# Optimization experiments

Hardware: AMD Instinct MI355X
Metric: run time of the kernel (lower is better)

Reference implementation:

```python
import jax, jax.numpy as jnp
import numpy as np

V = 30000   # vocab (from get_word_embedding default)
D = 640     # d_model
L = 6       # num_layers
H = 8       # num_heads
DH = D // H # head dim 80
FF = 4 * D  # ffn hidden 2560
BOS = 1
EOS = 2
LN_EPS = 1e-6


def _ln(x, s, b):
    m = x.mean(-1, keepdims=True)
    v = ((x - m) ** 2).mean(-1, keepdims=True)
    return (x - m) / jnp.sqrt(v + LN_EPS) * s + b


def _get_logits(tokens, seq_len, emb, Wq, bq, Wk, bk, Wv, bv, Wo, bo,
                ln1s, ln1b, W1, b1, W2, b2, ln2s, ln2b, lmW, lmb):
    # tokens: (B,S) int; seq_len: (B,) int
    B, S = tokens.shape
    h = emb[tokens]                                   # (B,S,D), no pos-enc / scaling in source
    look_ahead = jnp.triu(jnp.ones((S, S), jnp.float32), k=1)          # 1 = masked (TF-style)
    pad = (jnp.arange(S)[None, :] >= seq_len[:, None]).astype(jnp.float32)  # (B,S)
    mask = jnp.maximum(look_ahead[None, None, :, :], pad[:, None, None, :])  # (B,1,S,S)

    def layer(h, p):
        wq, bq_, wk, bk_, wv, bv_, wo, bo_, l1s, l1b, w1, b1_, w2, b2_, l2s, l2b = p
        q = (h @ wq + bq_).reshape(B, S, H, DH)
        k = (h @ wk + bk_).reshape(B, S, H, DH)
        v = (h @ wv + bv_).reshape(B, S, H, DH)
        scores = jnp.einsum('bqhd,bkhd->bhqk', q, k) / jnp.sqrt(jnp.float32(DH))
        scores = scores - mask * 1e9
        a = jax.nn.softmax(scores, axis=-1)
        o = jnp.einsum('bhqk,bkhd->bqhd', a, v).reshape(B, S, D) @ wo + bo_
        h = _ln(h + o, l1s, l1b)                      # post-LN residual
        f = jax.nn.relu(h @ w1 + b1_) @ w2 + b2_
        h = _ln(h + f, l2s, l2b)
        return h, None

    h, _ = jax.lax.scan(layer, h, (Wq, bq, Wk, bk, Wv, bv, Wo, bo,
                                   ln1s, ln1b, W1, b1, W2, b2, ln2s, ln2b))
    return h @ lmW + lmb                              # (B,S,V)


def setup_inputs() -> dict:
    key = jax.random.key(0)
    ks = jax.random.split(key, 12)
    std = 0.02

    def n(k, shape):
        return jax.random.normal(k, shape, jnp.float32) * std

    return {
        'initial_words': jax.random.randint(ks[0], (4, 8), 3, V, dtype=jnp.int32),
        'max_length': 32,
        'emb': n(ks[1], (V, D)),
        'Wq': n(ks[2], (L, D, D)), 'bq': jnp.zeros((L, D), jnp.float32),
        'Wk': n(ks[3], (L, D, D)), 'bk': jnp.zeros((L, D), jnp.float32),
        'Wv': n(ks[4], (L, D, D)), 'bv': jnp.zeros((L, D), jnp.float32),
        'Wo': n(ks[5], (L, D, D)), 'bo': jnp.zeros((L, D), jnp.float32),
        'ln1s': jnp.ones((L, D), jnp.float32), 'ln1b': jnp.zeros((L, D), jnp.float32),
        'W1': n(ks[6], (L, D, FF)), 'b1': jnp.zeros((L, FF), jnp.float32),
        'W2': n(ks[7], (L, FF, D)), 'b2': jnp.zeros((L, D), jnp.float32),
        'ln2s': jnp.ones((L, D), jnp.float32), 'ln2b': jnp.zeros((L, D), jnp.float32),
        'lmW': n(ks[8], (D, V)), 'lmb': jnp.zeros((V,), jnp.float32),
    }


def reference(initial_words, max_length, emb, Wq, bq, Wk, bk, Wv, bv, Wo, bo,
              ln1s, ln1b, W1, b1, W2, b2, ln2s, ln2b, lmW, lmb):
    B, init_len = initial_words.shape
    seq_len = jnp.full((B,), max_length, jnp.int32)
    S = max_length + 1  # BOS + max_length slots, as in the torch padding logic
    inp = (jnp.zeros((B, S), jnp.int32)
           .at[:, 0].set(BOS)
           .at[:, 1:1 + init_len].set(initial_words.astype(jnp.int32)))

    def cond(c):
        _inp, cl, tok = c
        return (cl + 1 <= max_length) & jnp.any(tok != EOS)

    def body(c):
        inp, cl, _tok = c
        logits = _get_logits(inp, seq_len, emb, Wq, bq, Wk, bk, Wv, bv, Wo, bo,
                             ln1s, ln1b, W1, b1, W2, b2, ln2s, ln2b, lmW, lmb)
        step_logits = jax.lax.dynamic_index_in_dim(logits, cl, axis=1, keepdims=False)
        tok = jnp.argmax(step_logits, axis=-1).astype(jnp.int32)
        inp = inp.at[:, cl + 1].set(tok)
        return (inp, cl + 1, tok)

    inp, _, _ = jax.lax.while_loop(
        cond, body,
        (inp, jnp.int32(init_len), jnp.full((B,), -100, jnp.int32)))
    return inp[:, 1:]
```

## Files before the change

kernel.cpp:

```cpp
#include <hip/hip_runtime.h>
#include <math.h>

#define B 4
#define SEQ 33
#define MAXLEN 32
#define D 640
#define NH 8
#define DH 80
#define NL 6
#define FF 2560
#define V 30000
#define INITLEN 8
#define NBLK 1024
#define NT 256
#define EOS_TOK 2
#define NPOS_P 9
#define NR_P 36
#define LM_NB 938

#define QKV_N 120
#define AW_B 120
#define RF_B 184
#define F1_B 188
#define F2_B 348
#define RQ_B 428

#define NFLAGS 1024
#define NSLOT 8
#define SLOT_U 16

typedef float f4 __attribute__((ext_vector_type(4)));

struct Par {
  const int* iw;
  const float* emb;
  const float *Wq, *bq, *Wk, *bk, *Wv, *bv, *Wo, *bo;
  const float *ln1s, *ln1b, *W1, *b1, *W2, *b2, *ln2s, *ln2b, *lmW, *lmb;
  int* out;
};

__device__ __align__(256) float g_Kc[(size_t)NL * B * NH * SEQ * DH];
__device__ __align__(256) float g_Vc[(size_t)NL * B * NH * SEQ * DH];
__device__ __align__(256) float g_x[B * D];
__device__ __align__(256) float g_h1[B * D];
__device__ __align__(256) float g_q[D * B];
__device__ __align__(256) float g_kcur[B * D];
__device__ __align__(256) float g_vcur[B * D];
__device__ __align__(256) float g_opart[NH * B * D];
__device__ __align__(256) float g_f1[B * FF];
__device__ __align__(256) float g_f2p[8 * D];
__device__ float g_xp[NR_P * D];
__device__ float g_h1p[NR_P * D];
__device__ float g_qkvpP[(size_t)8 * 1920 * NR_P];
__device__ float g_qP[(size_t)NH * NR_P * DH];
__device__ float g_opartP[(size_t)NH * D * NR_P];
__device__ float g_f1pP[(size_t)8 * FF * NR_P];
__device__ float g_f2pP[(size_t)32 * D * NR_P];
__device__ unsigned long long g_keys[(size_t)NBLK * B];
__device__ int g_tokens[B * SEQ];
__device__ int g_tok[B];
__device__ int g_stop;
__device__ unsigned g_flags[(size_t)NFLAGS * NSLOT * SLOT_U];
__device__ unsigned g_arrive = 0;
__device__ unsigned g_gen = 0;

#define KCIDX(l,b,h,pos,j) (((((size_t)(l)*B+(b))*NH+(h))*SEQ+(pos))*DH+(j))

__device__ __forceinline__ float ldc(const float* p) {
  return __hip_atomic_load(p, __ATOMIC_RELAXED, __HIP_MEMORY_SCOPE_AGENT);
}
__device__ __forceinline__ void stc(float* p, float v) {
  __hip_atomic_store(p, v, __ATOMIC_RELAXED, __HIP_MEMORY_SCOPE_AGENT);
}
__device__ __forceinline__ int ldci(const int* p) {
  return __hip_atomic_load(p, __ATOMIC_RELAXED, __HIP_MEMORY_SCOPE_AGENT);
}
__device__ __forceinline__ void stci(int* p, int v) {
  __hip_atomic_store(p, v, __ATOMIC_RELAXED, __HIP_MEMORY_SCOPE_AGENT);
}
__device__ __forceinline__ void stcu64(unsigned long long* p, unsigned long long v) {
  __hip_atomic_store(p, v, __ATOMIC_RELAXED, __HIP_MEMORY_SCOPE_AGENT);
}
__device__ __forceinline__ void st4c(float* p, f4 v) {
  asm volatile("global_store_dwordx4 %0, %1, off sc1" :: "v"(p), "v"(v) : "memory");
// ... 27 lines not shown
  __syncthreads();
}

__device__ __forceinline__ void stage_done(int idx) {
  asm volatile("s_waitcnt vmcnt(0)" ::: "memory");
  __syncthreads();
  if (threadIdx.x == 0) {
    __hip_atomic_fetch_add(
        &g_flags[((size_t)idx * NSLOT + (blockIdx.x & (NSLOT - 1))) * SLOT_U],
        1u, __ATOMIC_RELAXED, __HIP_MEMORY_SCOPE_AGENT);
  }
}

__device__ __forceinline__ void stage_wait(int idx, unsigned cnt) {
  if (threadIdx.x < 64) {
    const unsigned* base = &g_flags[(size_t)idx * NSLOT * SLOT_U];
    int spins = 0;
    for (;;) {
      unsigned v = 0u;
      if (threadIdx.x < NSLOT)
        v = __hip_atomic_load(base + (size_t)threadIdx.x * SLOT_U,
                              __ATOMIC_RELAXED, __HIP_MEMORY_SCOPE_AGENT);
      #pragma unroll
      for (int o = 4; o > 0; o >>= 1) v += __shfl_down(v, o, 64);
      v = __shfl(v, 0, 64);
      if (v >= cnt) break;
      if (spins < 16)      __builtin_amdgcn_s_sleep(1);
      else if (spins < 96) __builtin_amdgcn_s_sleep(16);
      else                 __builtin_amdgcn_s_sleep(127);
      ++spins;
    }
  }
  __syncthreads();
  asm volatile("" ::: "memory");
}

__device__ __forceinline__ float bred_sum(float v, float* s_red) {
  #pragma unroll
  for (int o = 32; o > 0; o >>= 1) v += __shfl_down(v, o, 64);
  __syncthreads();
  if ((threadIdx.x & 63) == 0) s_red[threadIdx.x >> 6] = v;
  __syncthreads();
  return s_red[0] + s_red[1] + s_red[2] + s_red[3];
}

__device__ void ln_inplace(float* row, const float* gam, const float* bet, float* s_red) {
  float ps = 0.f;
  for (int d = threadIdx.x; d < D; d += NT) ps += row[d];
  const float m = bred_sum(ps, s_red) * (1.0f / 640.0f);
  float pv = 0.f;
  for (int d = threadIdx.x; d < D; d += NT) { float t = row[d] - m; pv += t * t; }
  const float var = bred_sum(pv, s_red) * (1.0f / 640.0f);
  const float rstd = 1.0f / sqrtf(var + 1e-6f);
  for (int d = threadIdx.x; d < D; d += NT)
    row[d] = (row[d] - m) * rstd * gam[d] + bet[d];
  __syncthreads();
}


__device__ void st_QKV(const Par& p, int l, int t, float* s_x, float* s_t, float* s_r) {
  const int tid = threadIdx.x;
  const int cg = blockIdx.x;
  const int m = cg / 40, colm0 = (cg % 40) * 16;
  if (l == 0) {
    for (int i = tid; i < 640; i += NT) {
      const int b = i / 160, c4 = i % 160;
      const int tok = ldci(&g_tok[b]);
      *(f4*)&s_x[b * 640 + c4 * 4] = *(const f4*)&p.emb[(size_t)tok * D + c4 * 4];
    }
  } else {
    f4 xb[3];
    #pragma unroll
    for (int i = 0; i < 3; ++i) {
      const int idx = tid + i * NT;
      if (idx < 640) ld4c_issue(xb[i], &g_x[idx * 4]);
    }
    wait_vm();
    #pragma unroll
    for (int i = 0; i < 3; ++i) {
      const int idx = tid + i * NT;
      if (idx < 640) *(f4*)&s_x[idx * 4] = xb[i];
    }
  }
  __syncthreads();
  if (l == 0 && cg == 0) {
    for (int i = tid; i < 640; i += NT)
      st4c(&g_x[i * 4], *(f4*)&s_x[i * 4]);
  }
  const int ds = tid >> 4, c = tid & 15;
  const float* Wb = (m == 0 ? p.Wq : m == 1 ? p.Wk : p.Wv)
                    + (size_t)l * D * D + colm0 + c;
  float a0 = 0, a1 = 0, a2 = 0, a3 = 0;
  for (int kb = 0; kb < 40; kb += 8) {
    float w[8];
    #pragma unroll
    for (int j = 0; j < 8; ++j)
      w[j] = Wb[(size_t)(ds + (kb + j) * 16) * D];
    #pragma unroll
    for (int j = 0; j < 8; ++j) {
      const int dd = ds + (kb + j) * 16;
      a0 = fmaf(s_x[dd],        w[j], a0);
      a1 = fmaf(s_x[640 + dd],  w[j], a1);
      a2 = fmaf(s_x[1280 + dd], w[j], a2);
      a3 = fmaf(s_x[1920 + dd], w[j], a3);
    }
  }
  { f4 av = { a0, a1, a2, a3 }; *(f4*)&s_t[c * 68 + ds * 4] = av; }
  __syncthreads();
  if (tid < 64) {
    const int c2 = tid >> 2, b = tid & 3;
    float v = 0.f;
    #pragma unroll
    for (int d2 = 0; d2 < 16; ++d2) v += s_t[c2 * 68 + d2 * 4 + b];
    v += (m == 0 ? p.bq : m == 1 ? p.bk : p.bv)[(size_t)l * D + colm0 + c2];
    s_r[c2 * 4 + b] = v;
  }
  __syncthreads();
  if (m == 0) {
    if (tid < 16) {
      f4 v = { s_r[tid * 4], s_r[tid * 4 + 1], s_r[tid * 4 + 2], s_r[tid * 4 + 3] };
      st4c(&g_q[(size_t)(colm0 + tid) * 4], v);
    }
  } else {
    const int h = colm0 / 80, j0 = colm0 % 80;
    if (tid < 16) {
      const int cq = tid & 3, b = tid >> 2;
      f4 v = { s_r[(cq*4+0)*4+b], s_r[(cq*4+1)*4+b], s_r[(cq*4+2)*4+b], s_r[(cq*4+3)*4+b] };
      float* cache = (m == 1) ? g_Kc : g_Vc;
      st4c(&cache[KCIDX(l, b, h, t, j0 + cq * 4)], v);
      float* cur = (m == 1) ? g_kcur : g_vcur;
      st4c(&cur[b * D + colm0 + cq * 4], v);
    }
  }
}

__device__ void st_AW(const Par& p, int l, int pos,
                      float* s_q, float* s_k, float* s_v, float* s_o, float* s_sc, float* s_wo) {
  const int idx = blockIdx.x - AW_B, h = idx >> 3, c = idx & 7, tid = threadIdx.x;
  {
    f4 vq, vk, vv;
    if (tid < 80) {
      ld4c_issue(vq, &g_q[(size_t)(h * 80 + tid) * 4]);
      const int b = tid / 20, q4 = tid % 20;
      ld4c_issue(vk, &g_kcur[b * D + h * 80 + q4 * 4]);
      ld4c_issue(vv, &g_vcur[b * D + h * 80 + q4 * 4]);
    }
    wait_vm();
    if (tid < 80) {
      s_q[0*80+tid] = vq.x; s_q[80+tid] = vq.y; s_q[160+tid] = vq.z; s_q[240+tid] = vq.w;
      const int b = tid / 20, q4 = tid % 20;
      *(f4*)&s_k[b * 80 + q4 * 4] = vk;
      *(f4*)&s_v[b * 80 + q4 * 4] = vv;
    }
  }
  __syncthreads();
  const int nk = pos + 1;
  for (int task = tid; task < 4 * nk; task += NT) {
    const int b = task / nk, kp = task % nk;
    const float* qq = s_q + b * 80;
    float sd = 0.f;
    if (kp == pos) {
      const float* kk = s_k + b * 80;
      for (int j = 0; j < 80; ++j) sd += qq[j] * kk[j];
    } else {
      const f4* kk = (const f4*)&g_Kc[KCIDX(l, b, h, kp, 0)];
      #pragma unroll
      for (int j4 = 0; j4 < 20; ++j4) {
        f4 k4 = kk[j4];
        sd += qq[j4*4+0]*k4.x + qq[j4*4+1]*k4.y + qq[j4*4+2]*k4.z + qq[j4*4+3]*k4.w;
      }
    }
    s_sc[b * 33 + kp] = sd / 8.94427190999915878564f;
  }
  __syncthreads();
  if (tid < 4) {
    const int b = tid;
    float m = -1e30f;
    for (int k = 0; k < nk; ++k) m = fmaxf(m, s_sc[b * 33 + k]);
    float sum = 0.f;
    for (int k = 0; k < nk; ++k) { float e = expf(s_sc[b * 33 + k] - m); s_sc[b * 33 + k] = e; sum += e; }
    s_sc[132 + b] = 1.0f / sum;
  }
  __syncthreads();
  if (tid < 80) {
    const int b = tid / 20, j4 = tid % 20;
    f4 acc = { 0.f, 0.f, 0.f, 0.f };
    for (int kp = 0; kp < pos; ++kp) {
      f4 v = *(const f4*)&g_Vc[KCIDX(l, b, h, kp, j4 * 4)];
      const float wgt = s_sc[b * 33 + kp];
      acc.x += wgt * v.x; acc.y += wgt * v.y; acc.z += wgt * v.z; acc.w += wgt * v.w;
    }
    {
      f4 v = *(const f4*)&s_v[b * 80 + j4 * 4];
      const float wgt = s_sc[b * 33 + pos];
      acc.x += wgt * v.x; acc.y += wgt * v.y; acc.z += wgt * v.z; acc.w += wgt * v.w;
    }
    const float r = s_sc[132 + b];
    f4 o = { acc.x * r, acc.y * r, acc.z * r, acc.w * r };
    *(f4*)&s_o[b * 80 + j4 * 4] = o;
  }
  __syncthreads();
  if (tid < 240) {
    const int j = tid % 80, sub = tid / 80;
    const int col = c * 80 + j;
    const int d0 = sub * 27, d1 = (sub == 2) ? 80 : d0 + 27;
    const float* Wo = p.Wo + (size_t)l * D * D + col;
    float a0 = 0, a1 = 0, a2 = 0, a3 = 0;
    #pragma unroll 9
    for (int dd = d0; dd < d1; ++dd) {
      const float w = Wo[(size_t)(h * 80 + dd) * D];
      a0 += s_o[0*80+dd] * w; a1 += s_o[80+dd] * w;
      a2 += s_o[160+dd] * w; a3 += s_o[240+dd] * w;
    }
    float* tp = s_wo + (j * 3 + sub) * 4;
    tp[0] = a0; tp[1] = a1; tp[2] = a2; tp[3] = a3;
  }
  __syncthreads();
  if (tid < 80) {
    const int b = tid / 20, cq = tid % 20;
    f4 v;
    #pragma unroll
    for (int i = 0; i < 4; ++i) {
      const int j = cq * 4 + i;
      v[i] = s_wo[(j*3+0)*4+b] + s_wo[(j*3+1)*4+b] + s_wo[(j*3+2)*4+b];
    }
    st4c(&g_opart[((size_t)h * 4 + b) * D + c * 80 + cq * 4], v);
  }
}

__device__ void st_RF(const Par& p, int l, float* s_row, float* s_red) {
  const int b = blockIdx.x - RF_B, tid = threadIdx.x;
  f4 xv, ov[8];
  if (tid < 160) {
    ld4c_issue(xv, &g_x[b * D + tid * 4]);
    #pragma unroll
    for (int h = 0; h < 8; ++h)
      ld4c_issue(ov[h], &g_opart[((size_t)h * 4 + b) * D + tid * 4]);
  }
  wait_vm();
  if (tid < 160) {
    const float* bo = p.bo + (size_t)l * D + tid * 4;
    f4 a;
    a.x = xv.x + bo[0]; a.y = xv.y + bo[1]; a.z = xv.z + bo[2]; a.w = xv.w + bo[3];
    #pragma unroll
    for (int h = 0; h < 8; ++h) {
      a.x += ov[h].x; a.y += ov[h].y; a.z += ov[h].z; a.w += ov[h].w;
    }
    *(f4*)&s_row[tid * 4] = a;
  }
  __syncthreads();
  ln_inplace(s_row, p.ln1s + (size_t)l * D, p.ln1b + (size_t)l * D, s_red);
  if (tid < 160) st4c(&g_h1[b * D + tid * 4], *(f4*)&s_row[tid * 4]);
}

__device__ void st_F1(const Par& p, int l, float* s_x, float* s_t, float* s_r) {
  const int tid = threadIdx.x;
  const int cg = blockIdx.x - F1_B;
  const int col0 = cg * 16;
  f4 hb[3];
  #pragma unroll
  for (int i = 0; i < 3; ++i) {
    const int idx = tid + i * NT;
    if (idx < 640) ld4c_issue(hb[i], &g_h1[idx * 4]);
  }
  wait_vm();
  #pragma unroll
  for (int i = 0; i < 3; ++i) {
    const int idx = tid + i * NT;
    if (idx < 640) *(f4*)&s_x[idx * 4] = hb[i];
  }
  __syncthreads();
  const int ds = tid >> 4, c = tid & 15;
  const float* Wb = p.W1 + (size_t)l * D * FF + col0 + c;
  float a0 = 0, a1 = 0, a2 = 0, a3 = 0;
  for (int kb = 0; kb < 40; kb += 8) {
    float w[8];
    #pragma unroll
    for (int j = 0; j < 8; ++j)
      w[j] = Wb[(size_t)(ds + (kb + j) * 16) * FF];
    #pragma unroll
    for (int j = 0; j < 8; ++j) {
      const int dd = ds + (kb + j) * 16;
      a0 = fmaf(s_x[dd],        w[j], a0);
      a1 = fmaf(s_x[640 + dd],  w[j], a1);
      a2 = fmaf(s_x[1280 + dd], w[j], a2);
      a3 = fmaf(s_x[1920 + dd], w[j], a3);
    }
  }
  { f4 av = { a0, a1, a2, a3 }; *(f4*)&s_t[c * 68 + ds * 4] = av; }
  __syncthreads();
  if (tid < 64) {
    const int c2 = tid >> 2, b = tid & 3;
    float v = 0.f;
    #pragma unroll
    for (int d2 = 0; d2 < 16; ++d2) v += s_t[c2 * 68 + d2 * 4 + b];
    v += p.b1[(size_t)l * FF + col0 + c2];
    s_r[c2 * 4 + b] = fmaxf(v, 0.f);
  }
  __syncthreads();
  if (tid < 16) {
    const int cq = tid & 3, b = tid >> 2;
    f4 v = { s_r[(cq*4+0)*4+b], s_r[(cq*4+1)*4+b], s_r[(cq*4+2)*4+b], s_r[(cq*4+3)*4+b] };
    st4c(&g_f1[(size_t)b * FF + col0 + cq * 4], v);
  }
}

__device__ void st_F2(const Par& p, int l, float* s_f, float* s_t, float* s_r) {
  const int idx = blockIdx.x - F2_B, tid = threadIdx.x;
  const int hf = idx / 40, cg = idx % 40;
  const int col0 = cg * 16;
  f4 fb[5];
  #pragma unroll
  for (int i = 0; i < 5; ++i) {
    const int ii = tid + i * NT;
    const int b = ii / 320, fo = ii % 320;
    ld4c_issue(fb[i], &g_f1[(size_t)b * FF + hf * 1280 + fo * 4]);
  }
  wait_vm();
  #pragma unroll
  for (int i = 0; i < 5; ++i) {
    const int ii = tid + i * NT;
    const int b = ii / 320, fo = ii % 320;
    *(f4*)&s_f[b * 1280 + fo * 4] = fb[i];
  }
  __syncthreads();
  const int ds = tid >> 4, c = tid & 15;
  const float* Wb = p.W2 + (size_t)l * FF * D + (size_t)hf * 1280 * D + col0 + c;
  float a0 = 0, a1 = 0, a2 = 0, a3 = 0;
  for (int kb = 0; kb < 80; kb += 16) {
    float w[16];
    #pragma unroll
    for (int j = 0; j < 16; ++j)
      w[j] = Wb[(size_t)(ds + (kb + j) * 16) * D];
    #pragma unroll
    for (int j = 0; j < 16; ++j) {
      const int dl = ds + (kb + j) * 16;
      a0 = fmaf(s_f[dl],        w[j], a0);
      a1 = fmaf(s_f[1280 + dl], w[j], a1);
      a2 = fmaf(s_f[2560 + dl], w[j], a2);
      a3 = fmaf(s_f[3840 + dl], w[j], a3);
    }
  }
  { f4 av = { a0, a1, a2, a3 }; *(f4*)&s_t[c * 68 + ds * 4] = av; }
  __syncthreads();
  if (tid < 64) {
    const int c2 = tid >> 2, b = tid & 3;
    float v = 0.f;
    #pragma unroll
    for (int d2 = 0; d2 < 16; ++d2) v += s_t[c2 * 68 + d2 * 4 + b];
    s_r[c2 * 4 + b] = v;
  }
  __syncthreads();
  if (tid < 16) {
    const int cq = tid & 3, b = tid >> 2;
    f4 v = { s_r[(cq*4+0)*4+b], s_r[(cq*4+1)*4+b], s_r[(cq*4+2)*4+b], s_r[(cq*4+3)*4+b] };
    st4c(&g_f2p[((size_t)hf * 4 + b) * D + col0 + cq * 4], v);
  }
}

__device__ void st_RQ(const Par& p, int lprev, float* s_row, float* s_red) {
  const int b = blockIdx.x - RQ_B, tid = threadIdx.x;
  f4 hv, f0, f1v;
  if (tid < 160) {
    ld4c_issue(hv,  &g_h1[b * D + tid * 4]);
    ld4c_issue(f0,  &g_f2p[(size_t)(0 * 4 + b) * D + tid * 4]);
    ld4c_issue(f1v, &g_f2p[(size_t)(1 * 4 + b) * D + tid * 4]);
  }
  wait_vm();
  if (tid < 160) {
    const float* b2 = p.b2 + (size_t)lprev * D + tid * 4;
    f4 a;
    a.x = hv.x + f0.x + f1v.x + b2[0];
    a.y = hv.y + f0.y + f1v.y + b2[1];
    a.z = hv.z + f0.z + f1v.z + b2[2];
    a.w = hv.w + f0.w + f1v.w + b2[3];
    *(f4*)&s_row[tid * 4] = a;
  }
  __syncthreads();
  ln_inplace(s_row, p.ln2s + (size_t)lprev * D, p.ln2b + (size_t)lprev * D, s_red);
  if (tid < 160) st4c(&g_x[b * D + tid * 4], *(f4*)&s_row[tid * 4]);
}

__device__ void st_LM(const Par& p, float* s_xf, float* s_part, unsigned long long* s_key) {
  const int bid = blockIdx.x, tid = threadIdx.x;
  f4 xb[3];
  #pragma unroll
  for (int i = 0; i < 3; ++i) {
    const int idx = tid + i * NT;
    if (idx < 640) ld4c_issue(xb[i], &g_x[idx * 4]);
  }
  wait_vm();
  #pragma unroll
  for (int i = 0; i < 3; ++i) {
    const int idx = tid + i * NT;
    if (idx < 640) *(f4*)&s_xf[idx * 4] = xb[i];
  }
  __syncthreads();
  const int sg = tid >> 5, cj = tid & 31;
  const int col = bid * 32 + cj;
  float a0 = 0, a1 = 0, a2 = 0, a3 = 0;
  if (col < V) {
    const float* W = p.lmW + (size_t)sg * 80 * V + col;
    for (int kb = 0; kb < 80; kb += 16) {
      float w[16];
      #pragma unroll
      for (int j = 0; j < 16; ++j) w[j] = W[(size_t)(kb + j) * V];
      #pragma unroll
      for (int j = 0; j < 16; ++j) {
        const int d = sg * 80 + kb + j;
        a0 = fmaf(s_xf[d],        w[j], a0);
        a1 = fmaf(s_xf[640 + d],  w[j], a1);
        a2 = fmaf(s_xf[1280 + d], w[j], a2);
        a3 = fmaf(s_xf[1920 + d], w[j], a3);
      }
    }
  }
  float* t = s_part + (sg * 32 + cj) * 4;
  t[0] = a0; t[1] = a1; t[2] = a2; t[3] = a3;
  __syncthreads();
  if (tid < 128) {
    const int cj2 = tid >> 2, b = tid & 3, col2 = bid * 32 + cj2;
    unsigned long long key = 0ull;
    if (col2 < V) {
      float a = p.lmb[col2];
      #pragma unroll
      for (int sg2 = 0; sg2 < 8; ++sg2) a += s_part[(sg2 * 32 + cj2) * 4 + b];
      unsigned u = __float_as_uint(a);
      u = (u & 0x80000000u) ? ~u : (u | 0x80000000u);
      key = ((unsigned long long)u << 32) | (unsigned)(V - col2);
    }
    s_key[cj2 * 4 + b] = key;
  }
  __syncthreads();
  if (tid < 4) {
    unsigned long long k0 = 0ull;
    for (int cj2 = 0; cj2 < 32; ++cj2) {
      const unsigned long long k = s_key[cj2 * 4 + tid];
      if (k > k0) k0 = k;
    }
    stcu64(&g_keys[(size_t)bid * B + tid], k0);
  }
// ... 26 lines not shown
    s = mk64(kb3.x,kb3.y); if (s>m2) m2=s;  s = mk64(kb3.z,kb3.w); if (s>m3) m3=s;
  }
  #pragma unroll
  for (int o = 32; o > 0; o >>= 1) {
    unsigned long long s;
    s = __shfl_down(m0, o, 64); if (s > m0) m0 = s;
    s = __shfl_down(m1, o, 64); if (s > m1) m1 = s;
    s = __shfl_down(m2, o, 64); if (s > m2) m2 = s;
    s = __shfl_down(m3, o, 64); if (s > m3) m3 = s;
  }
  if ((tid & 63) == 0) {
    const int w = tid >> 6;
    s_k64[w * 4 + 0] = m0; s_k64[w * 4 + 1] = m1;
    s_k64[w * 4 + 2] = m2; s_k64[w * 4 + 3] = m3;
  }
  __syncthreads();
  if (tid == 0) {
    #pragma unroll
    for (int b = 0; b < B; ++b) {
      unsigned long long k0 = s_k64[b];
      #pragma unroll
      for (int w = 1; w < 4; ++w) if (s_k64[w * 4 + b] > k0) k0 = s_k64[w * 4 + b];
      const int tok = V - (int)(unsigned)(k0 & 0xFFFFFFFFull);
      stci(&g_tok[b], tok);
      stci(&g_tokens[b * SEQ + t + 1], tok);
      s_ctl[b] = tok;
    }
    int stop = (t == MAXLEN - 1) ? 1 : 0;
    if (s_ctl[0] == EOS_TOK && s_ctl[1] == EOS_TOK &&
        s_ctl[2] == EOS_TOK && s_ctl[3] == EOS_TOK) stop = 1;
    stci(&g_stop, stop);
  }
}


__device__ void st_Qp(const Par& p, int l, float* s_a) {
  const int idx = blockIdx.x, tid = threadIdx.x;
  const int h = idx / 24, rem = idx % 24, s = rem / 3, rg = rem % 3;
  const int r0 = rg * 12, d0 = s * 80;
  for (int i = tid; i < 960; i += NT) {
    const int ri = i / 80, dd = i % 80;
    s_a[i] = ldc(&g_xp[(r0 + ri) * D + d0 + dd]);
  }
  __syncthreads();
  if (tid < 240) {
    const int m = tid / 80, j = tid % 80, col = h * 80 + j;
    const float* W = (m == 0 ? p.Wq : m == 1 ? p.Wk : p.Wv) + (size_t)l * D * D + col;
    float acc[12];
    #pragma unroll
    for (int ri = 0; ri < 12; ++ri) acc[ri] = 0.f;
    for (int dd = 0; dd < 80; ++dd) {
      const float w = W[(size_t)(d0 + dd) * D];
      #pragma unroll
      for (int ri = 0; ri < 12; ++ri) acc[ri] += s_a[ri * 80 + dd] * w;
// ... 153 lines not shown
__device__ void st_RQp(const Par& p, int l, float* s_row, float* s_red) {
  const int r = blockIdx.x, tid = threadIdx.x;
  for (int col = tid; col < D; col += NT) {
    float a = ldc(&g_h1p[r * D + col]) + p.b2[(size_t)l * D + col];
    #pragma unroll 8
    for (int c = 0; c < 32; ++c) a += ldc(&g_f2pP[((size_t)c * D + col) * NR_P + r]);
    s_row[col] = a;
  }
  __syncthreads();
  ln_inplace(s_row, p.ln2s + (size_t)l * D, p.ln2b + (size_t)l * D, s_red);
  for (int col = tid; col < D; col += NT) stc(&g_xp[r * D + col], s_row[col]);
}

__device__ void st_RLp(const Par& p, float* s_row, float* s_red) {
  const int b = blockIdx.x, r = 32 + b, tid = threadIdx.x;
  for (int col = tid; col < D; col += NT) {
    float a = ldc(&g_h1p[r * D + col]) + p.b2[(size_t)(NL - 1) * D + col];
    #pragma unroll 8
    for (int c = 0; c < 32; ++c) a += ldc(&g_f2pP[((size_t)c * D + col) * NR_P + r]);
    s_row[col] = a;
  }
  __syncthreads();
  ln_inplace(s_row, p.ln2s + (size_t)(NL - 1) * D, p.ln2b + (size_t)(NL - 1) * D, s_red);
  for (int col = tid; col < D; col += NT) stc(&g_x[b * D + col], s_row[col]);
}

__global__ __launch_bounds__(NT, 4) void tfgen(Par p) {
  __shared__ float s_pool[6400];
  __shared__ float s_red[8];
  __shared__ unsigned long long s_key[128];
  __shared__ int s_ctl[8];

  const int bid = blockIdx.x, tid = threadIdx.x;
  int ep = 0;

  {
    unsigned* f = g_flags + (size_t)bid * NSLOT * SLOT_U;
    for (int i = tid; i < NSLOT * SLOT_U; i += NT) f[i] = 0u;
  }
  if (bid < NR_P) {
    const int pos = bid >> 2, b = bid & 3;
    const int tk = (pos == 0) ? 1 : p.iw[b * INITLEN + pos - 1];
    for (int d = tid; d < D; d += NT) stc(&g_xp[bid * D + d], p.emb[(size_t)tk * D + d]);
  }
  if (bid == NBLK - 1) {
    for (int i = tid; i < B * SEQ; i += NT) {
      const int b = i / SEQ, pos = i % SEQ;
// ... 16 lines not shown
    const int eA1 = ep++;
    if (bid >= 192 && bid < 224) { stage_wait(eQ, 192); st_AWp1(p, l); stage_done(eA1); }
    const int eA2 = ep++;
    if (bid >= 224 && bid < 256) { stage_wait(eA1, 32); st_AWp2(p, l, ps_a, ps_b, ps_c); stage_done(eA2); }
    const int eRF = ep++;
    if (bid < NR_P) { stage_wait(eA2, 32); st_RFp(p, l, ps_x, s_red); stage_done(eRF); }
    const int eF1 = ep++;
    if (bid < 240) { stage_wait(eRF, 36); st_F1p(p, l, ps_a); stage_done(eF1); }
    const int eF2 = ep++;
    if (bid >= 240 && bid < 336) { stage_wait(eF1, 240); st_F2p(p, l, ps_c); stage_done(eF2); }
    eF2last = eF2;
    if (l < NL - 1) {
      eRQ = ep++;
      if (bid < NR_P) { stage_wait(eF2, 96); st_RQp(p, l, ps_x, s_red); stage_done(eRQ); }
    }
  }

  for (int t = INITLEN;; ++t) {
    int eCTL;
    if (t == INITLEN) {
      const int eRLp = ep++;
      if (bid < 4) { stage_wait(eF2last, 96); st_RLp(p, s_pool, s_red); stage_done(eRLp); }
      const int eLM = ep++;
      if (bid < LM_NB) { stage_wait(eRLp, 4); st_LM(p, s_pool, s_pool + 2560, s_key); stage_done(eLM); }
      eCTL = ep++;
      if (bid == NBLK - 1) { stage_wait(eLM, LM_NB); st_CTL(t, s_key, s_ctl); stage_done(eCTL); }
    } else {
      int eRQd = -1, eF2s = -1;
      for (int l = 0; l < NL; ++l) {
        const int eQKV = ep++;
        if (bid < QKV_N) {
          if (l > 0) stage_wait(eRQd, 4);
          st_QKV(p, l, t, s_pool, s_pool + 2560, s_pool + 3648);
          stage_done(eQKV);
        }
        const int eAW = ep++;
        if (bid >= AW_B && bid < RF_B) {
          stage_wait(eQKV, QKV_N);
          st_AW(p, l, t, s_pool, s_pool + 320, s_pool + 640, s_pool + 960,
                s_pool + 1280, s_pool + 1440);
          stage_done(eAW);
        }
        const int eRF = ep++;
        if (bid >= RF_B && bid < F1_B) { stage_wait(eAW, 64); st_RF(p, l, s_pool, s_red); stage_done(eRF); }
        const int eF1 = ep++;
        if (bid >= F1_B && bid < F2_B) {
          stage_wait(eRF, 4);
          st_F1(p, l, s_pool, s_pool + 2560, s_pool + 3648);
          stage_done(eF1);
        }
        eF2s = ep++;
        if (bid >= F2_B && bid < RQ_B) {
          stage_wait(eF1, 160);
          st_F2(p, l, s_pool, s_pool + 5120, s_pool + 6208);
          stage_done(eF2s);
        }
        if (l < NL - 1) {
          eRQd = ep++;
          if (bid >= RQ_B && bid < RQ_B + 4) { stage_wait(eF2s, 80); st_RQ(p, l, s_pool, s_red); stage_done(eRQd); }
        }
      }
      const int eRL = ep++;
      if (bid >= RQ_B && bid < RQ_B + 4) { stage_wait(eF2s, 80); st_RQ(p, NL - 1, s_pool, s_red); stage_done(eRL); }
      const int eLM = ep++;
      if (bid < LM_NB) { stage_wait(eRL, 4); st_LM(p, s_pool, s_pool + 2560, s_key); stage_done(eLM); }
      eCTL = ep++;
      if (bid == NBLK - 1) { stage_wait(eLM, LM_NB); st_CTL(t, s_key, s_ctl); stage_done(eCTL); }
    }
    stage_wait(eCTL, 1);
    if (tid == 0) s_ctl[0] = ldci(&g_stop);
    __syncthreads();
    if (s_ctl[0]) break;
  }

  if (bid == 0) {
    for (int i = tid; i < B * MAXLEN; i += NT) {
      const int b = i >> 5, j = i & 31;
      p.out[i] = ldci(&g_tokens[b * SEQ + j + 1]);
    }
  }
}

extern "C" void kernel_launch(void* const* d_in, const int* in_sizes, int n_in,
                              void* d_out, int out_size, void* d_ws, size_t ws_size,
                              hipStream_t stream)
{
  (void)in_sizes; (void)n_in; (void)out_size; (void)d_ws; (void)ws_size;
  Par p;
  p.iw   = (const int*)  d_in[0];
  p.emb  = (const float*)d_in[2];
  p.Wq   = (const float*)d_in[3];  p.bq   = (const float*)d_in[4];
  p.Wk   = (const float*)d_in[5];  p.bk   = (const float*)d_in[6];
  p.Wv   = (const float*)d_in[7];  p.bv   = (const float*)d_in[8];
  p.Wo   = (const float*)d_in[9];  p.bo   = (const float*)d_in[10];
  p.ln1s = (const float*)d_in[11]; p.ln1b = (const float*)d_in[12];
// ... 14 lines not shown
```

Measured before the change: 18.13 ms.

## Version intermediate buffers per step and fold residual LayerNorm into QKV stage

Every intermediate activation buffer is now indexed by (step, layer), so no slot is reused across stages. Reads can then be plain loads instead of coherent atomic loads. The separate residual+LayerNorm (RQ) stage between layers is removed: each QKV block redoes the residual sum and LayerNorm itself, which drops one grid-wide stage wait per layer at the cost of redundant per-block work. The attention stage now reads the current K/V from the cache instead of separate buffers, flag slots grow to 32, and the weight-load unroll changes to 20. Plain loads on freshly written global data could read stale cached values if coherence is not guaranteed.

```diff
diff --git a/kernel.cpp b/kernel.cpp
--- a/kernel.cpp
+++ b/kernel.cpp
@@ -23,11 +23,13 @@
 #define RF_B 184
 #define F1_B 188
 #define F2_B 348
-#define RQ_B 428
+#define RL_B 428
 
 #define NFLAGS 1024
-#define NSLOT 8
+#define NSLOT 32
 #define SLOT_U 16
+
+#define VER(t,l) ((size_t)((t) * NL + (l)))
 
 typedef float f4 __attribute__((ext_vector_type(4)));
 
@@ -41,14 +43,15 @@
 
 __device__ __align__(256) float g_Kc[(size_t)NL * B * NH * SEQ * DH];
 __device__ __align__(256) float g_Vc[(size_t)NL * B * NH * SEQ * DH];
-__device__ __align__(256) float g_x[B * D];
-__device__ __align__(256) float g_h1[B * D];
-__device__ __align__(256) float g_q[D * B];
-__device__ __align__(256) float g_kcur[B * D];
-__device__ __align__(256) float g_vcur[B * D];
-__device__ __align__(256) float g_opart[NH * B * D];
-__device__ __align__(256) float g_f1[B * FF];
-__device__ __align__(256) float g_f2p[8 * D];
+__device__ __align__(256) float g_xv[(size_t)SEQ * NL * 2560];
+__device__ __align__(256) float g_h1v[(size_t)SEQ * NL * 2560];
+__device__ __align__(256) float g_qv[(size_t)SEQ * NL * 2560];
+__device__ __align__(256) float g_opartv[(size_t)SEQ * NL * 20480];
+__device__ __align__(256) float g_f1v[(size_t)SEQ * NL * 10240];
+__device__ __align__(256) float g_f2v[(size_t)SEQ * NL * 5120];
+__device__ __align__(256) float g_xlm[(size_t)SEQ * 2560];
+__device__ __align__(256) int   g_tokv[SEQ * 64];
+__device__ __align__(256) int   g_stopv[SEQ * 64];
 __device__ float g_xp[NR_P * D];
 __device__ float g_h1p[NR_P * D];
 __device__ float g_qkvpP[(size_t)8 * 1920 * NR_P];
@@ -58,8 +61,6 @@
 __device__ float g_f2pP[(size_t)32 * D * NR_P];
 __device__ unsigned long long g_keys[(size_t)NBLK * B];
 __device__ int g_tokens[B * SEQ];
-__device__ int g_tok[B];
-__device__ int g_stop;
 __device__ unsigned g_flags[(size_t)NFLAGS * NSLOT * SLOT_U];
 __device__ unsigned g_arrive = 0;
 __device__ unsigned g_gen = 0;
@@ -133,7 +134,7 @@
         v = __hip_atomic_load(base + (size_t)threadIdx.x * SLOT_U,
                               __ATOMIC_RELAXED, __HIP_MEMORY_SCOPE_AGENT);
       #pragma unroll
-      for (int o = 4; o > 0; o >>= 1) v += __shfl_down(v, o, 64);
+      for (int o = 16; o > 0; o >>= 1) v += __shfl_down(v, o, 64);
       v = __shfl(v, 0, 64);
       if (v >= cnt) break;
       if (spins < 16)      __builtin_amdgcn_s_sleep(1);
@@ -173,47 +174,63 @@
   const int tid = threadIdx.x;
   const int cg = blockIdx.x;
   const int m = cg / 40, colm0 = (cg % 40) * 16;
+  const int w = tid >> 6, lane = tid & 63;
   if (l == 0) {
-    for (int i = tid; i < 640; i += NT) {
-      const int b = i / 160, c4 = i % 160;
-      const int tok = ldci(&g_tok[b]);
-      *(f4*)&s_x[b * 640 + c4 * 4] = *(const f4*)&p.emb[(size_t)tok * D + c4 * 4];
-    }
+    const int tok = g_tokv[t * 64 + w];
+    for (int c4 = lane; c4 < 160; c4 += 64)
+      *(f4*)&s_x[w * 640 + c4 * 4] = *(const f4*)&p.emb[(size_t)tok * D + c4 * 4];
   } else {
-    f4 xb[3];
-    #pragma unroll
-    for (int i = 0; i < 3; ++i) {
-      const int idx = tid + i * NT;
-      if (idx < 640) ld4c_issue(xb[i], &g_x[idx * 4]);
-    }
-    wait_vm();
-    #pragma unroll
-    for (int i = 0; i < 3; ++i) {
-      const int idx = tid + i * NT;
-      if (idx < 640) *(f4*)&s_x[idx * 4] = xb[i];
-    }
-  }
-  __syncthreads();
-  if (l == 0 && cg == 0) {
+    const size_t ver = VER(t, l - 1);
+    const float* h1 = g_h1v + ver * 2560 + w * 640;
+    const float* fa = g_f2v + ver * 5120 + w * 640;
+    const float* fb = g_f2v + ver * 5120 + 2560 + w * 640;
+    const float* b2 = p.b2 + (size_t)(l - 1) * D;
+    for (int c4 = lane; c4 < 160; c4 += 64) {
+      f4 a = *(const f4*)&h1[c4 * 4];
+      f4 b = *(const f4*)&fa[c4 * 4];
+      f4 c = *(const f4*)&fb[c4 * 4];
+      const float* bb = b2 + c4 * 4;
+      f4 s = { a.x + b.x + c.x + bb[0], a.y + b.y + c.y + bb[1],
+               a.z + b.z + c.z + bb[2], a.w + b.w + c.w + bb[3] };
+      *(f4*)&s_x[w * 640 + c4 * 4] = s;
+    }
+    float ps = 0.f;
+    for (int i = lane; i < D; i += 64) ps += s_x[w * 640 + i];
+    #pragma unroll
+    for (int o = 32; o > 0; o >>= 1) ps += __shfl_xor(ps, o, 64);
+    const float mean = ps * (1.0f / 640.0f);
+    float pv = 0.f;
+    for (int i = lane; i < D; i += 64) { float d = s_x[w * 640 + i] - mean; pv += d * d; }
+    #pragma unroll
+    for (int o = 32; o > 0; o >>= 1) pv += __shfl_xor(pv, o, 64);
+    const float rstd = 1.0f / sqrtf(pv * (1.0f / 640.0f) + 1e-6f);
+    const float* gam = p.ln2s + (size_t)(l - 1) * D;
+    const float* bet = p.ln2b + (size_t)(l - 1) * D;
+    for (int i = lane; i < D; i += 64)
+      s_x[w * 640 + i] = (s_x[w * 640 + i] - mean) * rstd * gam[i] + bet[i];
+  }
+  __syncthreads();
+  if (cg == 0) {
+    const size_t xo = VER(t, l) * 2560;
     for (int i = tid; i < 640; i += NT)
-      st4c(&g_x[i * 4], *(f4*)&s_x[i * 4]);
+      st4c(&g_xv[xo + (size_t)i * 4], *(f4*)&s_x[i * 4]);
   }
   const int ds = tid >> 4, c = tid & 15;
   const float* Wb = (m == 0 ? p.Wq : m == 1 ? p.Wk : p.Wv)
                     + (size_t)l * D * D + colm0 + c;
   float a0 = 0, a1 = 0, a2 = 0, a3 = 0;
-  for (int kb = 0; kb < 40; kb += 8) {
-    float w[8];
-    #pragma unroll
-    for (int j = 0; j < 8; ++j)
-      w[j] = Wb[(size_t)(ds + (kb + j) * 16) * D];
-    #pragma unroll
-    for (int j = 0; j < 8; ++j) {
+  #pragma unroll
+  for (int kb = 0; kb < 40; kb += 20) {
+    float wv[20];
+    #pragma unroll
+    for (int j = 0; j < 20; ++j) wv[j] = Wb[(size_t)(ds + (kb + j) * 16) * D];
+    #pragma unroll
+    for (int j = 0; j < 20; ++j) {
       const int dd = ds + (kb + j) * 16;
-      a0 = fmaf(s_x[dd],        w[j], a0);
-      a1 = fmaf(s_x[640 + dd],  w[j], a1);
-      a2 = fmaf(s_x[1280 + dd], w[j], a2);
-      a3 = fmaf(s_x[1920 + dd], w[j], a3);
+      a0 = fmaf(s_x[dd],        wv[j], a0);
+      a1 = fmaf(s_x[640 + dd],  wv[j], a1);
+      a2 = fmaf(s_x[1280 + dd], wv[j], a2);
+      a3 = fmaf(s_x[1920 + dd], wv[j], a3);
     }
   }
   { f4 av = { a0, a1, a2, a3 }; *(f4*)&s_t[c * 68 + ds * 4] = av; }
@@ -230,7 +247,7 @@
   if (m == 0) {
     if (tid < 16) {
       f4 v = { s_r[tid * 4], s_r[tid * 4 + 1], s_r[tid * 4 + 2], s_r[tid * 4 + 3] };
-      st4c(&g_q[(size_t)(colm0 + tid) * 4], v);
+      st4c(&g_qv[VER(t, l) * 2560 + (size_t)(colm0 + tid) * 4], v);
     }
   } else {
     const int h = colm0 / 80, j0 = colm0 % 80;
@@ -239,47 +256,29 @@
       f4 v = { s_r[(cq*4+0)*4+b], s_r[(cq*4+1)*4+b], s_r[(cq*4+2)*4+b], s_r[(cq*4+3)*4+b] };
       float* cache = (m == 1) ? g_Kc : g_Vc;
       st4c(&cache[KCIDX(l, b, h, t, j0 + cq * 4)], v);
-      float* cur = (m == 1) ? g_kcur : g_vcur;
-      st4c(&cur[b * D + colm0 + cq * 4], v);
-    }
-  }
-}
-
-__device__ void st_AW(const Par& p, int l, int pos,
-                      float* s_q, float* s_k, float* s_v, float* s_o, float* s_sc, float* s_wo) {
+    }
+  }
+}
+
+__device__ void st_AW(const Par& p, int l, int t,
+                      float* s_q, float* s_sc, float* s_o, float* s_wo) {
   const int idx = blockIdx.x - AW_B, h = idx >> 3, c = idx & 7, tid = threadIdx.x;
-  {
-    f4 vq, vk, vv;
-    if (tid < 80) {
-      ld4c_issue(vq, &g_q[(size_t)(h * 80 + tid) * 4]);
-      const int b = tid / 20, q4 = tid % 20;
-      ld4c_issue(vk, &g_kcur[b * D + h * 80 + q4 * 4]);
-      ld4c_issue(vv, &g_vcur[b * D + h * 80 + q4 * 4]);
-    }
-    wait_vm();
-    if (tid < 80) {
-      s_q[0*80+tid] = vq.x; s_q[80+tid] = vq.y; s_q[160+tid] = vq.z; s_q[240+tid] = vq.w;
-      const int b = tid / 20, q4 = tid % 20;
-      *(f4*)&s_k[b * 80 + q4 * 4] = vk;
-      *(f4*)&s_v[b * 80 + q4 * 4] = vv;
-    }
-  }
-  __syncthreads();
-  const int nk = pos + 1;
+  const size_t qo = VER(t, l) * 2560;
+  if (tid < 80) {
+    f4 q = *(const f4*)&g_qv[qo + (size_t)(h * 80 + tid) * 4];
+    s_q[tid] = q.x; s_q[80 + tid] = q.y; s_q[160 + tid] = q.z; s_q[240 + tid] = q.w;
+  }
+  __syncthreads();
+  const int nk = t + 1;
   for (int task = tid; task < 4 * nk; task += NT) {
     const int b = task / nk, kp = task % nk;
     const float* qq = s_q + b * 80;
+    const f4* kk = (const f4*)&g_Kc[KCIDX(l, b, h, kp, 0)];
     float sd = 0.f;
-    if (kp == pos) {
-      const float* kk = s_k + b * 80;
-      for (int j = 0; j < 80; ++j) sd += qq[j] * kk[j];
-    } else {
-      const f4* kk = (const f4*)&g_Kc[KCIDX(l, b, h, kp, 0)];
-      #pragma unroll
-      for (int j4 = 0; j4 < 20; ++j4) {
-        f4 k4 = kk[j4];
-        sd += qq[j4*4+0]*k4.x + qq[j4*4+1]*k4.y + qq[j4*4+2]*k4.z + qq[j4*4+3]*k4.w;
-      }
+    #pragma unroll
+    for (int j4 = 0; j4 < 20; ++j4) {
+      f4 k4 = kk[j4];
+      sd += qq[j4*4+0]*k4.x + qq[j4*4+1]*k4.y + qq[j4*4+2]*k4.z + qq[j4*4+3]*k4.w;
     }
     s_sc[b * 33 + kp] = sd / 8.94427190999915878564f;
   }
@@ -296,14 +295,9 @@
   if (tid < 80) {
     const int b = tid / 20, j4 = tid % 20;
     f4 acc = { 0.f, 0.f, 0.f, 0.f };
-    for (int kp = 0; kp < pos; ++kp) {
+    for (int kp = 0; kp < nk; ++kp) {
       f4 v = *(const f4*)&g_Vc[KCIDX(l, b, h, kp, j4 * 4)];
       const float wgt = s_sc[b * 33 + kp];
-      acc.x += wgt * v.x; acc.y += wgt * v.y; acc.z += wgt * v.z; acc.w += wgt * v.w;
-    }
-    {
-      f4 v = *(const f4*)&s_v[b * 80 + j4 * 4];
-      const float wgt = s_sc[b * 33 + pos];
       acc.x += wgt * v.x; acc.y += wgt * v.y; acc.z += wgt * v.z; acc.w += wgt * v.w;
     }
     const float r = s_sc[132 + b];
@@ -335,67 +329,56 @@
       const int j = cq * 4 + i;
       v[i] = s_wo[(j*3+0)*4+b] + s_wo[(j*3+1)*4+b] + s_wo[(j*3+2)*4+b];
     }
-    st4c(&g_opart[((size_t)h * 4 + b) * D + c * 80 + cq * 4], v);
-  }
-}
-
-__device__ void st_RF(const Par& p, int l, float* s_row, float* s_red) {
+    st4c(&g_opartv[VER(t, l) * 20480 + (size_t)(h * 4 + b) * 640 + c * 80 + cq * 4], v);
+  }
+}
+
+__device__ void st_RF(const Par& p, int l, int t, float* s_row, float* s_red) {
   const int b = blockIdx.x - RF_B, tid = threadIdx.x;
-  f4 xv, ov[8];
+  const size_t ver = VER(t, l);
   if (tid < 160) {
-    ld4c_issue(xv, &g_x[b * D + tid * 4]);
-    #pragma unroll
-    for (int h = 0; h < 8; ++h)
-      ld4c_issue(ov[h], &g_opart[((size_t)h * 4 + b) * D + tid * 4]);
-  }
-  wait_vm();
-  if (tid < 160) {
+    f4 xv = *(const f4*)&g_xv[ver * 2560 + (size_t)b * 640 + tid * 4];
     const float* bo = p.bo + (size_t)l * D + tid * 4;
     f4 a;
     a.x = xv.x + bo[0]; a.y = xv.y + bo[1]; a.z = xv.z + bo[2]; a.w = xv.w + bo[3];
     #pragma unroll
     for (int h = 0; h < 8; ++h) {
-      a.x += ov[h].x; a.y += ov[h].y; a.z += ov[h].z; a.w += ov[h].w;
+      f4 ov = *(const f4*)&g_opartv[ver * 20480 + (size_t)(h * 4 + b) * 640 + tid * 4];
+      a.x += ov.x; a.y += ov.y; a.z += ov.z; a.w += ov.w;
     }
     *(f4*)&s_row[tid * 4] = a;
   }
   __syncthreads();
   ln_inplace(s_row, p.ln1s + (size_t)l * D, p.ln1b + (size_t)l * D, s_red);
-  if (tid < 160) st4c(&g_h1[b * D + tid * 4], *(f4*)&s_row[tid * 4]);
-}
-
-__device__ void st_F1(const Par& p, int l, float* s_x, float* s_t, float* s_r) {
+  if (tid < 160) st4c(&g_h1v[ver * 2560 + (size_t)b * 640 + tid * 4], *(f4*)&s_row[tid * 4]);
+}
+
+__device__ void st_F1(const Par& p, int l, int t, float* s_x, float* s_t, float* s_r) {
   const int tid = threadIdx.x;
   const int cg = blockIdx.x - F1_B;
   const int col0 = cg * 16;
-  f4 hb[3];
+  const size_t ver = VER(t, l);
   #pragma unroll
   for (int i = 0; i < 3; ++i) {
     const int idx = tid + i * NT;
-    if (idx < 640) ld4c_issue(hb[i], &g_h1[idx * 4]);
-  }
-  wait_vm();
-  #pragma unroll
-  for (int i = 0; i < 3; ++i) {
-    const int idx = tid + i * NT;
-    if (idx < 640) *(f4*)&s_x[idx * 4] = hb[i];
+    if (idx < 640) *(f4*)&s_x[idx * 4] = *(const f4*)&g_h1v[ver * 2560 + (size_t)idx * 4];
   }
   __syncthreads();
   const int ds = tid >> 4, c = tid & 15;
   const float* Wb = p.W1 + (size_t)l * D * FF + col0 + c;
   float a0 = 0, a1 = 0, a2 = 0, a3 = 0;
-  for (int kb = 0; kb < 40; kb += 8) {
-    float w[8];
-    #pragma unroll
-    for (int j = 0; j < 8; ++j)
-      w[j] = Wb[(size_t)(ds + (kb + j) * 16) * FF];
-    #pragma unroll
-    for (int j = 0; j < 8; ++j) {
+  #pragma unroll
+  for (int kb = 0; kb < 40; kb += 20) {
+    float wv[20];
+    #pragma unroll
+    for (int j = 0; j < 20; ++j) wv[j] = Wb[(size_t)(ds + (kb + j) * 16) * FF];
+    #pragma unroll
+    for (int j = 0; j < 20; ++j) {
       const int dd = ds + (kb + j) * 16;
-      a0 = fmaf(s_x[dd],        w[j], a0);
-      a1 = fmaf(s_x[640 + dd],  w[j], a1);
-      a2 = fmaf(s_x[1280 + dd], w[j], a2);
-      a3 = fmaf(s_x[1920 + dd], w[j], a3);
+      a0 = fmaf(s_x[dd],        wv[j], a0);
+      a1 = fmaf(s_x[640 + dd],  wv[j], a1);
+      a2 = fmaf(s_x[1280 + dd], wv[j], a2);
+      a3 = fmaf(s_x[1920 + dd], wv[j], a3);
     }
   }
   { f4 av = { a0, a1, a2, a3 }; *(f4*)&s_t[c * 68 + ds * 4] = av; }
@@ -412,44 +395,38 @@
   if (tid < 16) {
     const int cq = tid & 3, b = tid >> 2;
     f4 v = { s_r[(cq*4+0)*4+b], s_r[(cq*4+1)*4+b], s_r[(cq*4+2)*4+b], s_r[(cq*4+3)*4+b] };
-    st4c(&g_f1[(size_t)b * FF + col0 + cq * 4], v);
-  }
-}
-
-__device__ void st_F2(const Par& p, int l, float* s_f, float* s_t, float* s_r) {
+    st4c(&g_f1v[ver * 10240 + (size_t)b * 2560 + col0 + cq * 4], v);
+  }
+}
+
+__device__ void st_F2(const Par& p, int l, int t, float* s_f, float* s_t, float* s_r) {
   const int idx = blockIdx.x - F2_B, tid = threadIdx.x;
   const int hf = idx / 40, cg = idx % 40;
   const int col0 = cg * 16;
-  f4 fb[5];
+  const size_t ver = VER(t, l);
   #pragma unroll
   for (int i = 0; i < 5; ++i) {
     const int ii = tid + i * NT;
     const int b = ii / 320, fo = ii % 320;
-    ld4c_issue(fb[i], &g_f1[(size_t)b * FF + hf * 1280 + fo * 4]);
-  }
-  wait_vm();
-  #pragma unroll
-  for (int i = 0; i < 5; ++i) {
-    const int ii = tid + i * NT;
-    const int b = ii / 320, fo = ii % 320;
-    *(f4*)&s_f[b * 1280 + fo * 4] = fb[i];
+    *(f4*)&s_f[b * 1280 + fo * 4] =
+        *(const f4*)&g_f1v[ver * 10240 + (size_t)b * 2560 + hf * 1280 + fo * 4];
   }
   __syncthreads();
   const int ds = tid >> 4, c = tid & 15;
   const float* Wb = p.W2 + (size_t)l * FF * D + (size_t)hf * 1280 * D + col0 + c;
   float a0 = 0, a1 = 0, a2 = 0, a3 = 0;
-  for (int kb = 0; kb < 80; kb += 16) {
-    float w[16];
-    #pragma unroll
-    for (int j = 0; j < 16; ++j)
-      w[j] = Wb[(size_t)(ds + (kb + j) * 16) * D];
-    #pragma unroll
-    for (int j = 0; j < 16; ++j) {
+  #pragma unroll
+  for (int kb = 0; kb < 80; kb += 20) {
+    float wv[20];
+    #pragma unroll
+    for (int j = 0; j < 20; ++j) wv[j] = Wb[(size_t)(ds + (kb + j) * 16) * D];
+    #pragma unroll
+    for (int j = 0; j < 20; ++j) {
       const int dl = ds + (kb + j) * 16;
-      a0 = fmaf(s_f[dl],        w[j], a0);
-      a1 = fmaf(s_f[1280 + dl], w[j], a1);
-      a2 = fmaf(s_f[2560 + dl], w[j], a2);
-      a3 = fmaf(s_f[3840 + dl], w[j], a3);
+      a0 = fmaf(s_f[dl],        wv[j], a0);
+      a1 = fmaf(s_f[1280 + dl], wv[j], a1);
+      a2 = fmaf(s_f[2560 + dl], wv[j], a2);
+      a3 = fmaf(s_f[3840 + dl], wv[j], a3);
     }
   }
   { f4 av = { a0, a1, a2, a3 }; *(f4*)&s_t[c * 68 + ds * 4] = av; }
@@ -465,46 +442,37 @@
   if (tid < 16) {
     const int cq = tid & 3, b = tid >> 2;
     f4 v = { s_r[(cq*4+0)*4+b], s_r[(cq*4+1)*4+b], s_r[(cq*4+2)*4+b], s_r[(cq*4+3)*4+b] };
-    st4c(&g_f2p[((size_t)hf * 4 + b) * D + col0 + cq * 4], v);
-  }
-}
-
-__device__ void st_RQ(const Par& p, int lprev, float* s_row, float* s_red) {
-  const int b = blockIdx.x - RQ_B, tid = threadIdx.x;
-  f4 hv, f0, f1v;
+    st4c(&g_f2v[ver * 5120 + (size_t)(hf * 4 + b) * 640 + col0 + cq * 4], v);
+  }
+}
+
+__device__ void st_RL(const Par& p, int t, float* s_row, float* s_red) {
+  const int b = blockIdx.x - RL_B, tid = threadIdx.x;
+  const size_t ver = VER(t, NL - 1);
   if (tid < 160) {
-    ld4c_issue(hv,  &g_h1[b * D + tid * 4]);
-    ld4c_issue(f0,  &g_f2p[(size_t)(0 * 4 + b) * D + tid * 4]);
-    ld4c_issue(f1v, &g_f2p[(size_t)(1 * 4 + b) * D + tid * 4]);
-  }
-  wait_vm();
-  if (tid < 160) {
-    const float* b2 = p.b2 + (size_t)lprev * D + tid * 4;
+    f4 h  = *(const f4*)&g_h1v[ver * 2560 + (size_t)b * 640 + tid * 4];
+    f4 fa = *(const f4*)&g_f2v[ver * 5120 + (size_t)b * 640 + tid * 4];
+    f4 fb = *(const f4*)&g_f2v[ver * 5120 + 2560 + (size_t)b * 640 + tid * 4];
+    const float* b2 = p.b2 + (size_t)(NL - 1) * D + tid * 4;
     f4 a;
-    a.x = hv.x + f0.x + f1v.x + b2[0];
-    a.y = hv.y + f0.y + f1v.y + b2[1];
-    a.z = hv.z + f0.z + f1v.z + b2[2];
-    a.w = hv.w + f0.w + f1v.w + b2[3];
+    a.x = h.x + fa.x + fb.x + b2[0];
+    a.y = h.y + fa.y + fb.y + b2[1];
+    a.z = h.z + fa.z + fb.z + b2[2];
+    a.w = h.w + fa.w + fb.w + b2[3];
     *(f4*)&s_row[tid * 4] = a;
   }
   __syncthreads();
-  ln_inplace(s_row, p.ln2s + (size_t)lprev * D, p.ln2b + (size_t)lprev * D, s_red);
-  if (tid < 160) st4c(&g_x[b * D + tid * 4], *(f4*)&s_row[tid * 4]);
-}
-
-__device__ void st_LM(const Par& p, float* s_xf, float* s_part, unsigned long long* s_key) {
+  ln_inplace(s_row, p.ln2s + (size_t)(NL - 1) * D, p.ln2b + (size_t)(NL - 1) * D, s_red);
+  if (tid < 160)
+    st4c(&g_xlm[(size_t)t * 2560 + (size_t)b * 640 + tid * 4], *(f4*)&s_row[tid * 4]);
+}
+
+__device__ void st_LM(const Par& p, int t, float* s_xf, float* s_part, unsigned long long* s_key) {
   const int bid = blockIdx.x, tid = threadIdx.x;
-  f4 xb[3];
   #pragma unroll
   for (int i = 0; i < 3; ++i) {
     const int idx = tid + i * NT;
-    if (idx < 640) ld4c_issue(xb[i], &g_x[idx * 4]);
-  }
-  wait_vm();
-  #pragma unroll
-  for (int i = 0; i < 3; ++i) {
-    const int idx = tid + i * NT;
-    if (idx < 640) *(f4*)&s_xf[idx * 4] = xb[i];
+    if (idx < 640) *(f4*)&s_xf[idx * 4] = *(const f4*)&g_xlm[(size_t)t * 2560 + (size_t)idx * 4];
   }
   __syncthreads();
   const int sg = tid >> 5, cj = tid & 31;
@@ -512,12 +480,13 @@
   float a0 = 0, a1 = 0, a2 = 0, a3 = 0;
   if (col < V) {
     const float* W = p.lmW + (size_t)sg * 80 * V + col;
-    for (int kb = 0; kb < 80; kb += 16) {
-      float w[16];
-      #pragma unroll
-      for (int j = 0; j < 16; ++j) w[j] = W[(size_t)(kb + j) * V];
-      #pragma unroll
-      for (int j = 0; j < 16; ++j) {
+    #pragma unroll
+    for (int kb = 0; kb < 80; kb += 20) {
+      float w[20];
+      #pragma unroll
+      for (int j = 0; j < 20; ++j) w[j] = W[(size_t)(kb + j) * V];
+      #pragma unroll
+      for (int j = 0; j < 20; ++j) {
         const int d = sg * 80 + kb + j;
         a0 = fmaf(s_xf[d],        w[j], a0);
         a1 = fmaf(s_xf[640 + d],  w[j], a1);
@@ -526,8 +495,8 @@
       }
     }
   }
-  float* t = s_part + (sg * 32 + cj) * 4;
-  t[0] = a0; t[1] = a1; t[2] = a2; t[3] = a3;
+  float* tp = s_part + (sg * 32 + cj) * 4;
+  tp[0] = a0; tp[1] = a1; tp[2] = a2; tp[3] = a3;
   __syncthreads();
   if (tid < 128) {
     const int cj2 = tid >> 2, b = tid & 3, col2 = bid * 32 + cj2;
@@ -600,14 +569,14 @@
       #pragma unroll
       for (int w = 1; w < 4; ++w) if (s_k64[w * 4 + b] > k0) k0 = s_k64[w * 4 + b];
       const int tok = V - (int)(unsigned)(k0 & 0xFFFFFFFFull);
-      stci(&g_tok[b], tok);
       stci(&g_tokens[b * SEQ + t + 1], tok);
+      stci(&g_tokv[(t + 1) * 64 + b], tok);
       s_ctl[b] = tok;
     }
     int stop = (t == MAXLEN - 1) ? 1 : 0;
     if (s_ctl[0] == EOS_TOK && s_ctl[1] == EOS_TOK &&
         s_ctl[2] == EOS_TOK && s_ctl[3] == EOS_TOK) stop = 1;
-    stci(&g_stop, stop);
+    stci(&g_stopv[t * 64], stop);
   }
 }
 
@@ -807,7 +776,8 @@
   }
   __syncthreads();
   ln_inplace(s_row, p.ln2s + (size_t)(NL - 1) * D, p.ln2b + (size_t)(NL - 1) * D, s_red);
-  for (int col = tid; col < D; col += NT) stc(&g_x[b * D + col], s_row[col]);
+  for (int col = tid; col < D; col += NT)
+    stc(&g_xlm[(size_t)INITLEN * 2560 + (size_t)b * 640 + col], s_row[col]);
 }
 
 __global__ __launch_bounds__(NT, 4) void tfgen(Par p) {
@@ -870,55 +840,48 @@
       const int eRLp = ep++;
       if (bid < 4) { stage_wait(eF2last, 96); st_RLp(p, s_pool, s_red); stage_done(eRLp); }
       const int eLM = ep++;
-      if (bid < LM_NB) { stage_wait(eRLp, 4); st_LM(p, s_pool, s_pool + 2560, s_key); stage_done(eLM); }
+      if (bid < LM_NB) { stage_wait(eRLp, 4); st_LM(p, t, s_pool, s_pool + 2560, s_key); stage_done(eLM); }
       eCTL = ep++;
       if (bid == NBLK - 1) { stage_wait(eLM, LM_NB); st_CTL(t, s_key, s_ctl); stage_done(eCTL); }
     } else {
-      int eRQd = -1, eF2s = -1;
+      int eF2s = -1;
       for (int l = 0; l < NL; ++l) {
         const int eQKV = ep++;
         if (bid < QKV_N) {
-          if (l > 0) stage_wait(eRQd, 4);
+          if (l > 0) stage_wait(eF2s, 80);
           st_QKV(p, l, t, s_pool, s_pool + 2560, s_pool + 3648);
           stage_done(eQKV);
         }
         const int eAW = ep++;
         if (bid >= AW_B && bid < RF_B) {
           stage_wait(eQKV, QKV_N);
-          st_AW(p, l, t, s_pool, s_pool + 320, s_pool + 640, s_pool + 960,
-                s_pool + 1280, s_pool + 1440);
+          st_AW(p, l, t, s_pool, s_pool + 320, s_pool + 480, s_pool + 800);
           stage_done(eAW);
         }
         const int eRF = ep++;
-        if (bid >= RF_B && bid < F1_B) { stage_wait(eAW, 64); st_RF(p, l, s_pool, s_red); stage_done(eRF); }
+        if (bid >= RF_B && bid < F1_B) { stage_wait(eAW, 64); st_RF(p, l, t, s_pool, s_red); stage_done(eRF); }
         const int eF1 = ep++;
         if (bid >= F1_B && bid < F2_B) {
           stage_wait(eRF, 4);
-          st_F1(p, l, s_pool, s_pool + 2560, s_pool + 3648);
+          st_F1(p, l, t, s_pool, s_pool + 2560, s_pool + 3648);
           stage_done(eF1);
         }
         eF2s = ep++;
-        if (bid >= F2_B && bid < RQ_B) {
+        if (bid >= F2_B && bid < RL_B) {
           stage_wait(eF1, 160);
-          st_F2(p, l, s_pool, s_pool + 5120, s_pool + 6208);
+          st_F2(p, l, t, s_pool, s_pool + 5120, s_pool + 6208);
           stage_done(eF2s);
-        }
-        if (l < NL - 1) {
-          eRQd = ep++;
-          if (bid >= RQ_B && bid < RQ_B + 4) { stage_wait(eF2s, 80); st_RQ(p, l, s_pool, s_red); stage_done(eRQd); }
         }
       }
       const int eRL = ep++;
-      if (bid >= RQ_B && bid < RQ_B + 4) { stage_wait(eF2s, 80); st_RQ(p, NL - 1, s_pool, s_red); stage_done(eRL); }
+      if (bid >= RL_B && bid < RL_B + 4) { stage_wait(eF2s, 80); st_RL(p, t, s_pool, s_red); stage_done(eRL); }
       const int eLM = ep++;
-      if (bid < LM_NB) { stage_wait(eRL, 4); st_LM(p, s_pool, s_pool + 2560, s_key); stage_done(eLM); }
+      if (bid < LM_NB) { stage_wait(eRL, 4); st_LM(p, t, s_pool, s_pool + 2560, s_key); stage_done(eLM); }
       eCTL = ep++;
       if (bid == NBLK - 1) { stage_wait(eLM, LM_NB); st_CTL(t, s_key, s_ctl); stage_done(eCTL); }
     }
     stage_wait(eCTL, 1);
-    if (tid == 0) s_ctl[0] = ldci(&g_stop);
-    __syncthreads();
-    if (s_ctl[0]) break;
+    if (g_stopv[t * 64]) break;
   }
 
   if (bid == 0) {
```

Result: faster. 17.66 ms (-2.6%).
